# Optimization experiments

Hardware: AMD Instinct MI355X
Metric: run time of the kernel (lower is better)

Reference implementation:

```python
import jax, jax.numpy as jnp
import numpy as np

B, S, D = 64, 512, 1024


def setup_inputs() -> dict:
    key = jax.random.key(0)
    k_h, k_w = jax.random.split(key)
    last_hidden_state = jax.random.normal(k_h, (B, S, D), dtype=jnp.float32)
    # word_ids: sorted, contiguous subword->word indices per row (tokenizer word_ids).
    inc = jax.random.bernoulli(k_w, 0.5, (B, S)).astype(jnp.int32)
    inc = inc.at[:, 0].set(0)  # first token starts word 0
    word_ids = jnp.cumsum(inc, axis=1)  # [B, S], max ~ S/2 words
    return {"last_hidden_state": last_hidden_state, "word_ids": word_ids}


def reference(last_hidden_state, word_ids):
    # Faithful, vectorized version of merge_subword_representation:
    # out[i, w] = mean of last_hidden_state[i, t] over t with word_ids[i, t] == w,
    # for w in [0, tot_words_i); remaining positions keep original values.
    b, s, d = last_hidden_state.shape
    seg_sum = jax.vmap(
        lambda h, w: jax.ops.segment_sum(h, w, num_segments=s)
    )(last_hidden_state, word_ids)                                  # [B, S, D]
    cnt = jax.vmap(
        lambda w: jax.ops.segment_sum(jnp.ones((s,), last_hidden_state.dtype), w, num_segments=s)
    )(word_ids)                                                     # [B, S]
    means = seg_sum / jnp.maximum(cnt, 1.0)[..., None]              # safe: valid segments have cnt>=1
    tot_words = jnp.max(word_ids, axis=1) + 1                       # [B]
    pos = jnp.arange(s)
    write_mask = pos[None, :] < tot_words[:, None]                  # [B, S]
    return jnp.where(write_mask[..., None], means, last_hidden_state)
```

## Files before the change

kernel.cpp:

```cpp
#include <hip/hip_runtime.h>

#define BS 64
#define SS 512
#define DD 1024
#define WPB 8
#define NVEC (DD / 4)

typedef float f4 __attribute__((ext_vector_type(4)));

__global__ __launch_bounds__(256) void merge_subword_kernel(
    const float* __restrict__ h,
    const int*   __restrict__ wid,
    float*       __restrict__ out)
{
    const int chunk = blockIdx.x;
    const int b     = blockIdx.y;
    const int w0    = chunk * WPB;

    __shared__ int s_wid[SS];
    __shared__ int s_lo[WPB], s_hi[WPB];

    const int* row = wid + b * SS;
    for (int i = threadIdx.x; i < SS; i += 256) s_wid[i] = row[i];
    __syncthreads();

    if (threadIdx.x < WPB) {
        const int w = w0 + (int)threadIdx.x;
        int lo = 0, hi = SS;
        while (lo < hi) { int m = (lo + hi) >> 1; if (s_wid[m] < w) lo = m + 1; else hi = m; }
        s_lo[threadIdx.x] = lo;
        int lo2 = lo, hi2 = SS;
        while (lo2 < hi2) { int m = (lo2 + hi2) >> 1; if (s_wid[m] <= w) lo2 = m + 1; else hi2 = m; }
        s_hi[threadIdx.x] = lo2;
    }
    __syncthreads();

    const int tot = s_wid[SS - 1] + 1;
    const int tid = threadIdx.x;

    #pragma unroll
    for (int k = 0; k < WPB; ++k) {
        const int w = w0 + k;
        f4* dst = (f4*)(out + ((size_t)b * SS + w) * DD);
        if (w >= tot) {
            const f4* src = (const f4*)(h + ((size_t)b * SS + w) * DD);
            __builtin_nontemporal_store(src[tid], dst + tid);
        } else {
            const int lo = s_lo[k], hi = s_hi[k];
            const float inv = 1.0f / (float)(hi - lo);
            f4 acc = (f4)(0.f);
            const f4* base = (const f4*)(h + ((size_t)b * SS + lo) * DD);
            for (int t = 0; t < hi - lo; ++t) {
                acc += base[(size_t)t * NVEC + tid];
            }
            acc *= inv;
            __builtin_nontemporal_store(acc, dst + tid);
        }
    }
}

extern "C" void kernel_launch(void* const* d_in, const int* in_sizes, int n_in,
                              void* d_out, int out_size, void* d_ws, size_t ws_size,
                              hipStream_t stream) {
    (void)in_sizes; (void)n_in; (void)out_size; (void)d_ws; (void)ws_size;
    const float* h   = (const float*)d_in[0];
    const int*   wid = (const int*)d_in[1];
    float*       out = (float*)d_out;

    dim3 grid(SS / WPB, BS);
    dim3 block(256);
    merge_subword_kernel<<<grid, block, 0, stream>>>(h, wid, out);
}
```

Before: 58.10 us.

## Precompute word boundaries in separate kernel and launch one block per word

Adds a small prepass kernel that computes each word's start and length from the sorted word ids by detecting boundaries, packing both into a workspace array. The main kernel then launches one 256-thread block per (batch, word) instead of one block per eight words, dropping the shared-memory load and per-block binary searches. This raises block count eightfold for more parallelism on a memory-bound op, at the cost of an extra kernel launch and a dependent global read per block.

Result: faster. 56.54 us (-2.7%).

```diff
diff --git a/kernel.cpp b/kernel.cpp
--- a/kernel.cpp
+++ b/kernel.cpp
@@ -3,71 +3,77 @@
 #define BS 64
 #define SS 512
 #define DD 1024
-#define WPB 8
 #define NVEC (DD / 4)
 
 typedef float f4 __attribute__((ext_vector_type(4)));
 
+__global__ __launch_bounds__(512) void bounds_kernel(
+    const int* __restrict__ wid,
+    unsigned int* __restrict__ bounds)
+{
+    const int b = blockIdx.x;
+    const int t = threadIdx.x;
+    const int* row = wid + b * SS;
+
+    __shared__ int s_lo[SS + 1];
+    __shared__ int s_tot;
+
+    const int w_t  = row[t];
+    const int prev = (t == 0) ? -1 : row[t - 1];
+    if (t == SS - 1) { s_tot = w_t + 1; s_lo[w_t + 1] = SS; }
+    if (w_t != prev) s_lo[w_t] = t;
+    __syncthreads();
+
+    const int tot = s_tot;
+    unsigned int val;
+    if (t < tot) {
+        const int lo  = s_lo[t];
+        const int len = s_lo[t + 1] - lo;
+        val = (unsigned int)lo | ((unsigned int)len << 16);
+    } else {
+        val = 0xFFFFFFFFu;
+    }
+    bounds[b * SS + t] = val;
+}
+
 __global__ __launch_bounds__(256) void merge_subword_kernel(
     const float* __restrict__ h,
-    const int*   __restrict__ wid,
-    float*       __restrict__ out)
+    const unsigned int* __restrict__ bounds,
+    float* __restrict__ out)
 {
-    const int chunk = blockIdx.x;
-    const int b     = blockIdx.y;
-    const int w0    = chunk * WPB;
-
-    __shared__ int s_wid[SS];
-    __shared__ int s_lo[WPB], s_hi[WPB];
-
-    const int* row = wid + b * SS;
-    for (int i = threadIdx.x; i < SS; i += 256) s_wid[i] = row[i];
-    __syncthreads();
-
-    if (threadIdx.x < WPB) {
-        const int w = w0 + (int)threadIdx.x;
-        int lo = 0, hi = SS;
-        while (lo < hi) { int m = (lo + hi) >> 1; if (s_wid[m] < w) lo = m + 1; else hi = m; }
-        s_lo[threadIdx.x] = lo;
-        int lo2 = lo, hi2 = SS;
-        while (lo2 < hi2) { int m = (lo2 + hi2) >> 1; if (s_wid[m] <= w) lo2 = m + 1; else hi2 = m; }
-        s_hi[threadIdx.x] = lo2;
-    }
-    __syncthreads();
-
-    const int tot = s_wid[SS - 1] + 1;
+    const int w = blockIdx.x;
+    const int b = blockIdx.y;
+    const unsigned int bd = bounds[b * SS + w];
     const int tid = threadIdx.x;
 
-    #pragma unroll
-    for (int k = 0; k < WPB; ++k) {
-        const int w = w0 + k;
-        f4* dst = (f4*)(out + ((size_t)b * SS + w) * DD);
-        if (w >= tot) {
-            const f4* src = (const f4*)(h + ((size_t)b * SS + w) * DD);
-            __builtin_nontemporal_store(src[tid], dst + tid);
-        } else {
-            const int lo = s_lo[k], hi = s_hi[k];
-            const float inv = 1.0f / (float)(hi - lo);
-            f4 acc = (f4)(0.f);
-            const f4* base = (const f4*)(h + ((size_t)b * SS + lo) * DD);
-            for (int t = 0; t < hi - lo; ++t) {
-                acc += base[(size_t)t * NVEC + tid];
-            }
-            acc *= inv;
-            __builtin_nontemporal_store(acc, dst + tid);
+    f4* dst = (f4*)(out + ((size_t)b * SS + w) * DD);
+
+    if (bd == 0xFFFFFFFFu) {
+        const f4* src = (const f4*)(h + ((size_t)b * SS + w) * DD);
+        __builtin_nontemporal_store(src[tid], dst + tid);
+    } else {
+        const int lo  = (int)(bd & 0xFFFFu);
+        const int len = (int)(bd >> 16);
+        const float inv = 1.0f / (float)len;
+        f4 acc = (f4)(0.f);
+        const f4* base = (const f4*)(h + ((size_t)b * SS + lo) * DD);
+        for (int t = 0; t < len; ++t) {
+            acc += base[(size_t)t * NVEC + tid];
         }
+        acc *= inv;
+        __builtin_nontemporal_store(acc, dst + tid);
     }
 }
 
 extern "C" void kernel_launch(void* const* d_in, const int* in_sizes, int n_in,
                               void* d_out, int out_size, void* d_ws, size_t ws_size,
                               hipStream_t stream) {
-    (void)in_sizes; (void)n_in; (void)out_size; (void)d_ws; (void)ws_size;
+    (void)in_sizes; (void)n_in; (void)out_size; (void)ws_size;
     const float* h   = (const float*)d_in[0];
     const int*   wid = (const int*)d_in[1];
     float*       out = (float*)d_out;
+    unsigned int* bounds = (unsigned int*)d_ws;
 
-    dim3 grid(SS / WPB, BS);
-    dim3 block(256);
-    merge_subword_kernel<<<grid, block, 0, stream>>>(h, wid, out);
+    bounds_kernel<<<dim3(BS), dim3(SS), 0, stream>>>(wid, bounds);
+    merge_subword_kernel<<<dim3(SS, BS), dim3(256), 0, stream>>>(h, bounds, out);
 }
```
